# Kernel tuning notes

Hardware: AMD Instinct MI355X
Metric: run time of the kernel (lower is better)

## Reference

```python
import jax, jax.numpy as jnp
import numpy as np

N = 4096; E = 4096
IN_DIM = 256; H1 = 128; H2 = 128; H3 = 64; OUT = 16
NH1 = 2; NH2 = 2; ALPHA = 0.2
TDIMS = [933, 303, 683, 798]  # per-timepoint raw dims (nomal_linear1..4)
TP = 4; GRU_IN = 2 * OUT; GRU_H = 128


def _leaky(x, s):
    return jnp.where(x >= 0, x, s * x)


def _att_layer(x, mask, W, a, b):
    # GAT-style: h = xW; e = leaky(Wh1 + Wh2^T); adjacency-masked softmax; aggregate
    h = x @ W                                   # [N, d]
    d = W.shape[-1]
    e = _leaky((h @ a[:d])[:, None] + (h @ a[d:])[None, :], ALPHA)  # [N, N]
    att = jax.nn.softmax(jnp.where(mask, e, -9e15), axis=1)
    out = _leaky(att @ h, ALPHA)
    out = out / jnp.maximum(jnp.linalg.norm(out, axis=1, keepdims=True), 1e-12)
    return out + b

_multi_head = jax.vmap(_att_layer, in_axes=(None, None, 0, 0, 0))


def _encode(x, mask, W1, a1, b1, W2, a2, b2):
    x = jax.nn.elu(jnp.mean(_multi_head(x, mask, W1, a1, b1), axis=0))
    # second conv layer runs under torch.no_grad() in the original
    return jax.lax.stop_gradient(jnp.mean(_multi_head(x, mask, W2, a2, b2), axis=0))


def _gru_layer(xs, wih, whh, bih, bhh):
    # xs: [T, B, in]; torch GRU gate order (r, z, n)
    B = xs.shape[1]
    def step(h, xt):
        gi = xt @ wih + bih
        gh = h @ whh + bhh
        ir, iz, inn = jnp.split(gi, 3, axis=-1)
        hr, hz, hn = jnp.split(gh, 3, axis=-1)
        r = jax.nn.sigmoid(ir + hr)
        z = jax.nn.sigmoid(iz + hz)
        n = jnp.tanh(inn + r * hn)
        h_new = (1.0 - z) * n + z * h
        return h_new, h_new
    _, ys = jax.lax.scan(step, jnp.zeros((B, GRU_H), xs.dtype), xs)
    return ys


def setup_inputs() -> dict:
    key = jax.random.key(0)
    ks = iter(jax.random.split(key, 80))
    def rn(shape, s=0.05):
        return jax.random.normal(next(ks), shape, dtype=jnp.float32) * s
    inp = {}
    for i, d in enumerate(TDIMS):
        inp['x%d' % i] = rn((N, d), 1.0)
    inp['adj'] = jax.random.randint(next(ks), (N, N), 0, 2, dtype=jnp.int32)
    inp['train_sample'] = jax.random.randint(next(ks), (E, 2), 0, N)
    for i, d in enumerate(TDIMS):
        inp['nw%d' % i] = rn((d, IN_DIM))
        inp['nb%d' % i] = jnp.zeros((IN_DIM,), jnp.float32)
    inp['W1'] = rn((NH1, IN_DIM, H1)); inp['a1'] = rn((NH1, 2 * H1)); inp['b1'] = jnp.zeros((NH1, H1), jnp.float32)
    inp['W2'] = rn((NH2, H1, H2));     inp['a2'] = rn((NH2, 2 * H2)); inp['b2'] = jnp.zeros((NH2, H2), jnp.float32)
    inp['tfw1'] = rn((H2, H3)); inp['tfb1'] = jnp.zeros((H3,), jnp.float32)
    inp['tfw2'] = rn((H3, OUT)); inp['tfb2'] = jnp.zeros((OUT,), jnp.float32)
    inp['tgw1'] = rn((H2, H3)); inp['tgb1'] = jnp.zeros((H3,), jnp.float32)
    inp['tgw2'] = rn((H3, OUT)); inp['tgb2'] = jnp.zeros((OUT,), jnp.float32)
    inp['wih0'] = rn((GRU_IN, 3 * GRU_H)); inp['whh0'] = rn((GRU_H, 3 * GRU_H))
    inp['bih0'] = jnp.zeros((3 * GRU_H,), jnp.float32); inp['bhh0'] = jnp.zeros((3 * GRU_H,), jnp.float32)
    inp['wih1'] = rn((GRU_H, 3 * GRU_H)); inp['whh1'] = rn((GRU_H, 3 * GRU_H))
    inp['bih1'] = jnp.zeros((3 * GRU_H,), jnp.float32); inp['bhh1'] = jnp.zeros((3 * GRU_H,), jnp.float32)
    inp['attw'] = rn((GRU_H, GRU_H)); inp['attb'] = jnp.zeros((GRU_H,), jnp.float32)
    inp['fow'] = rn((GRU_H, 1)); inp['fob'] = jnp.zeros((1,), jnp.float32)
    return inp


def reference(x0, x1, x2, x3, adj, train_sample,
              nw0, nb0, nw1, nb1, nw2, nb2, nw3, nb3,
              W1, a1, b1, W2, a2, b2,
              tfw1, tfb1, tfw2, tfb2, tgw1, tgb1, tgw2, tgb2,
              wih0, whh0, bih0, bhh0, wih1, whh1, bih1, bhh1,
              attw, attb, fow, fob):
    mask = adj > 0
    xs = (x0, x1, x2, x3)
    nws = ((nw0, nb0), (nw1, nb1), (nw2, nb2), (nw3, nb3))
    tf_idx = train_sample[:, 0]
    tg_idx = train_sample[:, 1]
    steps = []
    for i in range(TP):  # fixed small loop over time points
        w, b = nws[i]
        e = xs[i] @ w + b                       # per-timepoint projection to input_dim
        embed = _encode(e, mask, W1, a1, b1, W2, a2, b2)
        # dropout (p=0.01) treated as identity for a deterministic reference
        tf = _leaky(_leaky(embed @ tfw1 + tfb1, 0.01) @ tfw2 + tfb2, 0.01)
        tg = _leaky(_leaky(embed @ tgw1 + tgb1, 0.01) @ tgw2 + tgb2, 0.01)
        steps.append(jnp.concatenate([tf[tf_idx], tg[tg_idx]], axis=1))  # [E, 32]
    h_x = jnp.stack(steps, axis=0)              # [T, E, 32]
    y0 = _gru_layer(h_x, wih0, whh0, bih0, bhh0)            # [T, E, 128]
    r_out = jnp.transpose(_gru_layer(y0, wih1, whh1, bih1, bhh1), (1, 0, 2))  # [E, T, 128]
    aw = jax.nn.softmax(r_out @ attw + attb, axis=1)        # softmax over time dim
    att_out = jnp.sum(aw * r_out, axis=1)                   # [E, 128]
    return att_out @ fow + fob                              # [E, 1]
```

## Files before the change

### kernel.cpp

```cpp
#include <hip/hip_runtime.h>
#include <cstdint>
#include <cstddef>

#define NN 4096
#define DH 128
#define TP 4
#define ATT_S 4
#define ATT_BM 64

typedef _Float16 f16x8 __attribute__((ext_vector_type(8)));
typedef float f32x4 __attribute__((ext_vector_type(4)));

__global__ __launch_bounds__(256) void pack_mask_k(const int* __restrict__ adj,
                                                   unsigned long long* __restrict__ mb) {
  int w = blockIdx.x * 4 + (threadIdx.x >> 6);
  int lane = threadIdx.x & 63;
  int v = adj[(size_t)w * 64 + lane];
  unsigned long long bits = __ballot(v > 0);
  if (lane == 0) mb[w] = bits;
}

template <int ACT, int BHEAD>
__global__ __launch_bounds__(256) void gemm_mfma_k(const float* __restrict__ A, const float* __restrict__ B,
                                                   const float* __restrict__ bias, float* __restrict__ C,
                                                   int M, int N, int K) {
  __shared__ _Float16 AH[64 * 64], AL[64 * 64];
  __shared__ _Float16 BH[64 * 64], BL[64 * 64];
  const int tid = threadIdx.x;
  const int bm = blockIdx.y * 64, bn = blockIdx.x * 64;
  const int arow = tid >> 2, akc = (tid & 3) * 16;
  const int bcol = tid & 63, bkc = (tid >> 6) * 16;
  const int w = tid >> 6, lane = tid & 63;
  const int wm = w >> 1, wn = w & 1;
  const int l15 = lane & 15, l4 = lane >> 4;
  f32x4 acc[2][2] = {};

  const float* Bp = B;
  int bcb = bn;
  if (BHEAD) { int hd = bn >> 7; Bp = B + (size_t)hd * K * 128; bcb = bn & 127; }
  const int ldb = BHEAD ? 128 : N;

  for (int k0 = 0; k0 < K; k0 += 64) {
    __syncthreads();
    {
      const float* ar = A + (size_t)(bm + arow) * K;
      f16x8 hv[2], lv[2];
#pragma unroll
      for (int e = 0; e < 16; e++) {
        int gk = k0 + akc + e;
        float v = (gk < K) ? ar[gk] : 0.f;
        _Float16 hi = (_Float16)v;
        hv[e >> 3][e & 7] = hi;
        lv[e >> 3][e & 7] = (_Float16)(v - (float)hi);
      }
#pragma unroll
      for (int hf = 0; hf < 2; hf++) {
        int byt = ((arow * 64 + akc + hf * 8) * 2) ^ ((arow & 7) << 4);
        *(f16x8*)((char*)AH + byt) = hv[hf];
        *(f16x8*)((char*)AL + byt) = lv[hf];
      }
    }
    {
      f16x8 hv[2], lv[2];
      const bool cok = (bcb + bcol) < ldb;
#pragma unroll
      for (int e = 0; e < 16; e++) {
        int gk = k0 + bkc + e;
        float v = (gk < K && cok) ? Bp[(size_t)gk * ldb + bcb + bcol] : 0.f;
        _Float16 hi = (_Float16)v;
        hv[e >> 3][e & 7] = hi;
        lv[e >> 3][e & 7] = (_Float16)(v - (float)hi);
      }
#pragma unroll
      for (int hf = 0; hf < 2; hf++) {
        int byt = ((bcol * 64 + bkc + hf * 8) * 2) ^ ((bcol & 7) << 4);
        *(f16x8*)((char*)BH + byt) = hv[hf];
        *(f16x8*)((char*)BL + byt) = lv[hf];
      }
    }
    __syncthreads();
#pragma unroll
    for (int kf = 0; kf < 2; kf++) {
      f16x8 ah[2], al[2], bh[2], bl[2];
#pragma unroll
      for (int m2 = 0; m2 < 2; m2++) {
        int r = wm * 32 + m2 * 16 + l15;
        int byt = ((r * 64 + kf * 32 + l4 * 8) * 2) ^ ((r & 7) << 4);
        ah[m2] = *(const f16x8*)((const char*)AH + byt);
        al[m2] = *(const f16x8*)((const char*)AL + byt);
      }
#pragma unroll
      for (int nf = 0; nf < 2; nf++) {
        int c = wn * 32 + nf * 16 + l15;
        int byt = ((c * 64 + kf * 32 + l4 * 8) * 2) ^ ((c & 7) << 4);
        bh[nf] = *(const f16x8*)((const char*)BH + byt);
        bl[nf] = *(const f16x8*)((const char*)BL + byt);
      }
#pragma unroll
      for (int m2 = 0; m2 < 2; m2++)
#pragma unroll
        for (int nf = 0; nf < 2; nf++) {
          acc[m2][nf] = __builtin_amdgcn_mfma_f32_16x16x32_f16(ah[m2], bh[nf], acc[m2][nf], 0, 0, 0);
          acc[m2][nf] = __builtin_amdgcn_mfma_f32_16x16x32_f16(ah[m2], bl[nf], acc[m2][nf], 0, 0, 0);
          acc[m2][nf] = __builtin_amdgcn_mfma_f32_16x16x32_f16(al[m2], bh[nf], acc[m2][nf], 0, 0, 0);
        }
    }
  }
#pragma unroll
  for (int m2 = 0; m2 < 2; m2++)
#pragma unroll
    for (int nf = 0; nf < 2; nf++) {
      int c = bn + wn * 32 + nf * 16 + l15;
      if (c < N) {
        float bv = bias ? bias[c] : 0.f;
#pragma unroll
        for (int q = 0; q < 4; q++) {
          int r = bm + wm * 32 + m2 * 16 + l4 * 4 + q;
          float v = acc[m2][nf][q] + bv;
          if (ACT == 1) v = (v >= 0.f) ? v : 0.01f * v;
          C[(size_t)r * N + c] = v;
        }
      }
    }
}

__global__ __launch_bounds__(256) void eler_k(const float* __restrict__ hcat, const float* __restrict__ a,
                                              float* __restrict__ el, float* __restrict__ er) {
  int head = blockIdx.y;
  const float* ah = a + (size_t)head * 256;
  int row = blockIdx.x * 4 + (threadIdx.x >> 6);
  int lane = threadIdx.x & 63;
  const float* hr = hcat + (size_t)row * 256 + head * 128;
  float h0 = hr[lane], h1 = hr[lane + 64];
  float pe = h0 * ah[lane] + h1 * ah[lane + 64];
  float pr = h0 * ah[128 + lane] + h1 * ah[192 + lane];
#pragma unroll
  for (int off = 32; off >= 1; off >>= 1) {
    pe += __shfl_xor(pe, off, 64);
    pr += __shfl_xor(pr, off, 64);
  }
  if (lane == 0) { el[(size_t)head * NN + row] = pe; er[(size_t)head * NN + row] = pr; }
}

__global__ __launch_bounds__(256) void rowmax_k(const float* __restrict__ el, const float* __restrict__ er,
                                                const unsigned long long* __restrict__ mb,
                                                float* __restrict__ mrow) {
  int head = blockIdx.y;
  int row = blockIdx.x * 4 + (threadIdx.x >> 6);
  int lane = threadIdx.x & 63;
  const float* erh = er + (size_t)head * NN;
  const unsigned long long* mr = mb + (size_t)row * 64;
  float mx = -INFINITY;
  for (int i = 0; i < 64; i++) {
    unsigned long long w = mr[i];
    float v = erh[i * 64 + lane];
    mx = fmaxf(mx, ((w >> lane) & 1ull) ? v : -INFINITY);
  }
#pragma unroll
  for (int off = 32; off >= 1; off >>= 1) mx = fmaxf(mx, __shfl_xor(mx, off, 64));
  if (lane == 0) {
    float s = el[(size_t)head * NN + row] + mx;
    mrow[(size_t)head * NN + row] = fmaxf(s, 0.2f * s);
  }
}

__global__ __launch_bounds__(256) void hsplit_k(const float* __restrict__ hcat,
                                                _Float16* __restrict__ HTH, _Float16* __restrict__ HTL) {
  const int jblk = blockIdx.x;
  const int head = blockIdx.y;
  const int tid = threadIdx.x;
  const int c = tid & 127;
  const size_t tileBase = ((size_t)head * (NN / 64) + jblk) * 8192;
#pragma unroll
  for (int kq = 0; kq < 4; kq++) {
    int k0 = (tid >> 7) * 32 + kq * 8;
    f16x8 hv, lv;
#pragma unroll
    for (int e = 0; e < 8; e++) {
      float v = hcat[(size_t)(jblk * 64 + k0 + e) * 256 + head * 128 + c];
      _Float16 hi = (_Float16)v;
      hv[e] = hi;
      lv[e] = (_Float16)(v - (float)hi);
    }
    int byt = ((c * 64 + k0) * 2) ^ ((c & 7) << 4);
    *(f16x8*)((char*)(HTH + tileBase) + byt) = hv;
    *(f16x8*)((char*)(HTL + tileBase) + byt) = lv;
  }
}

__global__ __launch_bounds__(256) void gat_mfma_k(const _Float16* __restrict__ HTH_g,
                                                  const _Float16* __restrict__ HTL_g,
                                                  const float* __restrict__ el, const float* __restrict__ er,
                                                  const float* __restrict__ mrow,
                                                  const unsigned long long* __restrict__ mb,
                                                  float* __restrict__ Opart, float* __restrict__ Zpart) {
  const int split = blockIdx.x;
  const int mblk = blockIdx.y;
  const int head = blockIdx.z;
  const float* elh = el + (size_t)head * NN;
  const float* erh = er + (size_t)head * NN;
  const float* mh = mrow + (size_t)head * NN;
  float* Op = Opart + ((size_t)head * ATT_S + split) * NN * DH;
  float* Zp = Zpart + ((size_t)head * ATT_S + split) * NN;

  __shared__ _Float16 PH[ATT_BM * 64];
  __shared__ _Float16 PL[ATT_BM * 64];
  __shared__ _Float16 HH[128 * 64];
  __shared__ _Float16 HL[128 * 64];
  __shared__ float zred[ATT_BM][4];

  const int tid = threadIdx.x;
  const int prow = tid >> 2;
  const int pk0 = (tid & 3) * 16;
  const int grow = mblk * ATT_BM + prow;
  const float el_r = elh[grow];
  const float m_r = mh[grow];
  const int w = tid >> 6, lane = tid & 63;
  const int wm = w >> 1, wn = w & 1;
  const int l15 = lane & 15, l4 = lane >> 4;

  f32x4 acc[2][4] = {};
  float zacc = 0.f;
  const int jbase = split * (NN / ATT_S);

  for (int jt = 0; jt < NN / ATT_S; jt += 64) {
    const int j0 = jbase + jt;
    const int jblk = j0 >> 6;
    const char* srcH = (const char*)(HTH_g + ((size_t)head * (NN / 64) + jblk) * 8192);
    const char* srcL = (const char*)(HTL_g + ((size_t)head * (NN / 64) + jblk) * 8192);
    __syncthreads();

    f16x8 rh[4], rl[4];
#pragma unroll
    for (int i = 0; i < 4; i++) {
      rh[i] = *(const f16x8*)(srcH + (tid + i * 256) * 16);
      rl[i] = *(const f16x8*)(srcL + (tid + i * 256) * 16);
    }

    {
      unsigned long long wbits = mb[(size_t)grow * 64 + jblk];
      float er_v[16];
#pragma unroll
      for (int q = 0; q < 4; q++) {
        float4 t = *(const float4*)&erh[j0 + pk0 + q * 4];
        er_v[q * 4 + 0] = t.x; er_v[q * 4 + 1] = t.y;
        er_v[q * 4 + 2] = t.z; er_v[q * 4 + 3] = t.w;
      }
      f16x8 hv[2], lv[2];
#pragma unroll
      for (int e = 0; e < 16; e++) {
        float sr = el_r + er_v[e];
        float s = fmaxf(sr, 0.2f * sr);
        float p = ((wbits >> (pk0 + e)) & 1ull) ? __expf(s - m_r) : 0.f;
        zacc += p;
        _Float16 hi = (_Float16)p;
        hv[e >> 3][e & 7] = hi;
        lv[e >> 3][e & 7] = (_Float16)(p - (float)hi);
      }
#pragma unroll
      for (int half = 0; half < 2; half++) {
        int byt = (((prow * 64) + pk0 + half * 8) * 2) ^ ((prow & 7) << 4);
        *(f16x8*)((char*)PH + byt) = hv[half];
        *(f16x8*)((char*)PL + byt) = lv[half];
      }
    }

#pragma unroll
    for (int i = 0; i < 4; i++) {
      *(f16x8*)((char*)HH + (tid + i * 256) * 16) = rh[i];
      *(f16x8*)((char*)HL + (tid + i * 256) * 16) = rl[i];
    }
    __syncthreads();

#pragma unroll
    for (int kf = 0; kf < 2; kf++) {
      f16x8 ah[2], al[2];
#pragma unroll
      for (int m2 = 0; m2 < 2; m2++) {
        int ar = wm * 32 + m2 * 16 + l15;
        int ak = kf * 32 + l4 * 8;
        int ab = ((ar * 64 + ak) * 2) ^ ((ar & 7) << 4);
        ah[m2] = *(const f16x8*)((const char*)PH + ab);
        al[m2] = *(const f16x8*)((const char*)PL + ab);
      }
#pragma unroll
      for (int nf = 0; nf < 4; nf++) {
        int bc = wn * 64 + nf * 16 + l15;
        int bk = kf * 32 + l4 * 8;
        int bb = ((bc * 64 + bk) * 2) ^ ((bc & 7) << 4);
        f16x8 bh = *(const f16x8*)((const char*)HH + bb);
        f16x8 bl = *(const f16x8*)((const char*)HL + bb);
#pragma unroll
        for (int m2 = 0; m2 < 2; m2++) {
          acc[m2][nf] = __builtin_amdgcn_mfma_f32_16x16x32_f16(ah[m2], bh, acc[m2][nf], 0, 0, 0);
          acc[m2][nf] = __builtin_amdgcn_mfma_f32_16x16x32_f16(ah[m2], bl, acc[m2][nf], 0, 0, 0);
          acc[m2][nf] = __builtin_amdgcn_mfma_f32_16x16x32_f16(al[m2], bh, acc[m2][nf], 0, 0, 0);
        }
      }
    }
  }

  zred[prow][tid & 3] = zacc;
  __syncthreads();
  if (tid < ATT_BM) {
    float z = zred[tid][0] + zred[tid][1] + zred[tid][2] + zred[tid][3];
    Zp[mblk * ATT_BM + tid] = z;
  }

#pragma unroll
  for (int m2 = 0; m2 < 2; m2++)
#pragma unroll
    for (int nf = 0; nf < 4; nf++)
#pragma unroll
      for (int q = 0; q < 4; q++) {
        int r = mblk * ATT_BM + wm * 32 + m2 * 16 + l4 * 4 + q;
        int c = wn * 64 + nf * 16 + l15;
        Op[(size_t)r * DH + c] = acc[m2][nf][q];
      }
}

template <int DO_ELU>
__global__ __launch_bounds__(256) void combine_k(const float* __restrict__ Opart,
                                                 const float* __restrict__ Zpart,
                                                 const float* __restrict__ bvec,
                                                 float* __restrict__ out) {
  int row = blockIdx.x * 4 + (threadIdx.x >> 6);
  int lane = threadIdx.x & 63;
  int c = lane * 2;
  float o0 = 0.f, o1 = 0.f;
#pragma unroll
  for (int hd = 0; hd < 2; hd++) {
    float a0 = 0.f, a1 = 0.f, Z = 0.f;
#pragma unroll
    for (int s = 0; s < ATT_S; s++) {
      const float* Op = Opart + ((size_t)hd * ATT_S + s) * NN * DH;
      float2 t = *(const float2*)&Op[(size_t)row * DH + c];
      a0 += t.x; a1 += t.y;
      Z += Zpart[((size_t)hd * ATT_S + s) * NN + row];
    }
    float invZ = 1.f / Z;
    float v0 = a0 * invZ, v1 = a1 * invZ;
    v0 = fmaxf(v0, 0.2f * v0);
    v1 = fmaxf(v1, 0.2f * v1);
    float ss = v0 * v0 + v1 * v1;
#pragma unroll
    for (int off = 32; off >= 1; off >>= 1) ss += __shfl_xor(ss, off, 64);
    float sc_ = 1.f / fmaxf(sqrtf(ss), 1e-12f);
    o0 += 0.5f * (v0 * sc_ + bvec[hd * DH + c]);
    o1 += 0.5f * (v1 * sc_ + bvec[hd * DH + c + 1]);
  }
  if (DO_ELU) {
    o0 = (o0 > 0.f) ? o0 : expm1f(o0);
    o1 = (o1 > 0.f) ? o1 : expm1f(o1);
  }
  float2 st = {o0, o1};
  *(float2*)&out[(size_t)row * DH + c] = st;
}

__global__ __launch_bounds__(256) void gather_k(const float* __restrict__ tf, const float* __restrict__ tg,
                                                const int* __restrict__ ts, float* __restrict__ hx_t) {
  int idx = blockIdx.x * 256 + threadIdx.x;
  int e = idx >> 5, c = idx & 31;
  int src = (c < 16) ? ts[e * 2] : ts[e * 2 + 1];
  float v = (c < 16) ? tf[(size_t)src * 16 + c] : tg[(size_t)src * 16 + (c - 16)];
  hx_t[idx] = v;
}

__global__ __launch_bounds__(256) void gru_gate_k(const float* __restrict__ gi, const float* __restrict__ gh,
                                                  const float* __restrict__ hprev, float* __restrict__ hout) {
  int idx = blockIdx.x * 256 + threadIdx.x;
  int b = idx >> 7, c = idx & 127;
  const float* gib = gi + (size_t)b * 384;
  const float* ghb = gh + (size_t)b * 384;
  float ir = gib[c], iz = gib[128 + c], in_ = gib[256 + c];
  float hr = ghb[c], hz = ghb[128 + c], hn = ghb[256 + c];
  float rr = 1.f / (1.f + __expf(-(ir + hr)));
  float zz = 1.f / (1.f + __expf(-(iz + hz)));
  float nn_ = tanhf(in_ + rr * hn);
  hout[idx] = (1.f - zz) * nn_ + zz * hprev[idx];
}

__global__ __launch_bounds__(256) void gru_gate0_k(const float* __restrict__ gi, const float* __restrict__ bhh,
                                                   float* __restrict__ hout) {
  int idx = blockIdx.x * 256 + threadIdx.x;
  int b = idx >> 7, c = idx & 127;
  const float* gib = gi + (size_t)b * 384;
  float ir = gib[c], iz = gib[128 + c], in_ = gib[256 + c];
  float hr = bhh[c], hz = bhh[128 + c], hn = bhh[256 + c];
  float rr = 1.f / (1.f + __expf(-(ir + hr)));
  float zz = 1.f / (1.f + __expf(-(iz + hz)));
  float nn_ = tanhf(in_ + rr * hn);
  hout[idx] = (1.f - zz) * nn_;
}

__global__ __launch_bounds__(256) void attpool_k(const float* __restrict__ z, const float* __restrict__ y,
                                                 float* __restrict__ o) {
  int idx = blockIdx.x * 256 + threadIdx.x;
  const size_t S = (size_t)NN * DH;
  float z0 = z[idx], z1 = z[idx + S], z2 = z[idx + 2 * S], z3 = z[idx + 3 * S];
  float mx = fmaxf(fmaxf(z0, z1), fmaxf(z2, z3));
  float e0 = __expf(z0 - mx), e1 = __expf(z1 - mx), e2 = __expf(z2 - mx), e3 = __expf(z3 - mx);
  float inv = 1.f / (e0 + e1 + e2 + e3);
  o[idx] = (e0 * y[idx] + e1 * y[idx + S] + e2 * y[idx + 2 * S] + e3 * y[idx + 3 * S]) * inv;
}

__global__ __launch_bounds__(256) void final_k(const float* __restrict__ at, const float* __restrict__ fow,
                                               const float* __restrict__ fob, float* __restrict__ out) {
  int row = blockIdx.x * 4 + (threadIdx.x >> 6);
  int lane = threadIdx.x & 63;
  const float* ar = at + (size_t)row * DH;
  float p = ar[lane] * fow[lane] + ar[lane + 64] * fow[lane + 64];
#pragma unroll
  for (int off = 32; off >= 1; off >>= 1) p += __shfl_xor(p, off, 64);
  if (lane == 0) out[row] = p + fob[0];
}

static inline void run_gemm(int act, const float* A, const float* B, const float* bias, float* C,
                            int M, int N, int K, hipStream_t s) {
  dim3 g((N + 63) / 64, M / 64), b(256);
  if (act == 0) gemm_mfma_k<0, 0><<<g, b, 0, s>>>(A, B, bias, C, M, N, K);
  else          gemm_mfma_k<1, 0><<<g, b, 0, s>>>(A, B, bias, C, M, N, K);
}
static inline void run_proj(const float* A, const float* B, float* C, int K, hipStream_t s) {
  gemm_mfma_k<0, 1><<<dim3(4, NN / 64), 256, 0, s>>>(A, B, nullptr, C, NN, 256, K);
}

extern "C" void kernel_launch(void* const* d_in, const int* in_sizes, int n_in,
                              void* d_out, int out_size, void* d_ws, size_t ws_size,
                              hipStream_t stream) {
  const float* x[4]  = {(const float*)d_in[0], (const float*)d_in[1], (const float*)d_in[2], (const float*)d_in[3]};
  const int* adj     = (const int*)d_in[4];
  const int* tsample = (const int*)d_in[5];
  const float* nw[4] = {(const float*)d_in[6], (const float*)d_in[8], (const float*)d_in[10], (const float*)d_in[12]};
  const float* nb[4] = {(const float*)d_in[7], (const float*)d_in[9], (const float*)d_in[11], (const float*)d_in[13]};
  const float* W1 = (const float*)d_in[14];
  const float* a1 = (const float*)d_in[15];
  const float* b1 = (const float*)d_in[16];
  const float* W2 = (const float*)d_in[17];
  const float* a2 = (const float*)d_in[18];
  const float* b2 = (const float*)d_in[19];
  const float* tfw1 = (const float*)d_in[20]; const float* tfb1 = (const float*)d_in[21];
  const float* tfw2 = (const float*)d_in[22]; const float* tfb2 = (const float*)d_in[23];
  const float* tgw1 = (const float*)d_in[24]; const float* tgb1 = (const float*)d_in[25];
  const float* tgw2 = (const float*)d_in[26]; const float* tgb2 = (const float*)d_in[27];
  const float* wih0 = (const float*)d_in[28]; const float* whh0 = (const float*)d_in[29];
  const float* bih0 = (const float*)d_in[30]; const float* bhh0 = (const float*)d_in[31];
  const float* wih1 = (const float*)d_in[32]; const float* whh1 = (const float*)d_in[33];
  const float* bih1 = (const float*)d_in[34]; const float* bhh1 = (const float*)d_in[35];
  const float* attw = (const float*)d_in[36]; const float* attb = (const float*)d_in[37];
  const float* fow  = (const float*)d_in[38]; const float* fob  = (const float*)d_in[39];
  float* out = (float*)d_out;

  char* base = (char*)d_ws;
  size_t off = 0;
  auto alloc = [&](size_t bytes) -> void* {
    void* p = base + off;
    off += (bytes + 255) & ~(size_t)255;
    return p;
  };
  const size_t SN = (size_t)NN * DH;
  unsigned long long* mbits = (unsigned long long*)alloc((size_t)NN * 64 * 8);
  float* ebuf = (float*)alloc((size_t)NN * 256 * 4);
  float* hcat = (float*)alloc((size_t)NN * 256 * 4);
  float* el   = (float*)alloc((size_t)2 * NN * 4);
  float* er   = (float*)alloc((size_t)2 * NN * 4);
  float* mrowb= (float*)alloc((size_t)2 * NN * 4);
  float* bufA = (float*)alloc(SN * 4);
  float* bufB = (float*)alloc(SN * 4);
  float* tmp1 = (float*)alloc((size_t)NN * 64 * 4);
  float* tfb_ = (float*)alloc((size_t)NN * 16 * 4);
  float* tgb_ = (float*)alloc((size_t)NN * 16 * 4);
  float* hx   = (float*)alloc((size_t)TP * NN * 32 * 4);
  float* y0   = (float*)alloc((size_t)TP * SN * 4);
  float* y1   = (float*)alloc((size_t)TP * SN * 4);
  float* gi   = (float*)alloc((size_t)NN * 384 * 4);
  float* gh   = (float*)alloc((size_t)NN * 384 * 4);
  float* Opart = y0;
  float* Zpart = gi;
  float* zatt   = gi;
  float* attout = hcat;
  _Float16* HTH = (_Float16*)ebuf;
  _Float16* HTL = HTH + (size_t)2 * NN * 128;

  const int TD[4] = {933, 303, 683, 798};

  pack_mask_k<<<(NN * 64) / 4, 256, 0, stream>>>(adj, mbits);

  for (int t = 0; t < TP; t++) {
    run_gemm(0, x[t], nw[t], nb[t], ebuf, NN, 256, TD[t], stream);

    run_proj(ebuf, W1, hcat, 256, stream);
    hsplit_k<<<dim3(NN / 64, 2), 256, 0, stream>>>(hcat, HTH, HTL);
    eler_k<<<dim3(NN / 4, 2), 256, 0, stream>>>(hcat, a1, el, er);
    rowmax_k<<<dim3(NN / 4, 2), 256, 0, stream>>>(el, er, mbits, mrowb);
    gat_mfma_k<<<dim3(ATT_S, NN / ATT_BM, 2), 256, 0, stream>>>(HTH, HTL, el, er, mrowb, mbits, Opart, Zpart);
    combine_k<1><<<NN / 4, 256, 0, stream>>>(Opart, Zpart, b1, bufB);

    run_proj(bufB, W2, hcat, 128, stream);
    hsplit_k<<<dim3(NN / 64, 2), 256, 0, stream>>>(hcat, HTH, HTL);
    eler_k<<<dim3(NN / 4, 2), 256, 0, stream>>>(hcat, a2, el, er);
    rowmax_k<<<dim3(NN / 4, 2), 256, 0, stream>>>(el, er, mbits, mrowb);
    gat_mfma_k<<<dim3(ATT_S, NN / ATT_BM, 2), 256, 0, stream>>>(HTH, HTL, el, er, mrowb, mbits, Opart, Zpart);
    combine_k<0><<<NN / 4, 256, 0, stream>>>(Opart, Zpart, b2, bufA);

    run_gemm(1, bufA, tfw1, tfb1, tmp1, NN, 64, DH, stream);
    run_gemm(1, tmp1, tfw2, tfb2, tfb_, NN, 16, 64, stream);
    run_gemm(1, bufA, tgw1, tgb1, tmp1, NN, 64, DH, stream);
    run_gemm(1, tmp1, tgw2, tgb2, tgb_, NN, 16, 64, stream);
    gather_k<<<(NN * 32) / 256, 256, 0, stream>>>(tfb_, tgb_, tsample, hx + (size_t)t * NN * 32);
  }

  run_gemm(0, hx, wih0, bih0, gi, NN, 384, 32, stream);
  gru_gate0_k<<<(int)(SN / 256), 256, 0, stream>>>(gi, bhh0, y0);
  for (int t = 1; t < TP; t++) {
    const float* hprev = y0 + (size_t)(t - 1) * SN;
    run_gemm(0, hx + (size_t)t * NN * 32, wih0, bih0, gi, NN, 384, 32, stream);
    run_gemm(0, hprev, whh0, bhh0, gh, NN, 384, DH, stream);
    gru_gate_k<<<(int)(SN / 256), 256, 0, stream>>>(gi, gh, hprev, y0 + (size_t)t * SN);
  }
  run_gemm(0, y0, wih1, bih1, gi, NN, 384, DH, stream);
  gru_gate0_k<<<(int)(SN / 256), 256, 0, stream>>>(gi, bhh1, y1);
  for (int t = 1; t < TP; t++) {
    const float* hprev = y1 + (size_t)(t - 1) * SN;
    run_gemm(0, y0 + (size_t)t * SN, wih1, bih1, gi, NN, 384, DH, stream);
    run_gemm(0, hprev, whh1, bhh1, gh, NN, 384, DH, stream);
    gru_gate_k<<<(int)(SN / 256), 256, 0, stream>>>(gi, gh, hprev, y1 + (size_t)t * SN);
  }

  run_gemm(0, y1, attw, attb, zatt, TP * NN, DH, DH, stream);
  attpool_k<<<(int)(SN / 256), 256, 0, stream>>>(zatt, y1, attout);
  final_k<<<NN / 4, 256, 0, stream>>>(attout, fow, fob, out);
}
```

Before: 1.356 ms.

## Split-K input projection GEMM and halve GAT attention row tile

The per-timepoint input projection (K up to 933) now runs as a split-K GEMM over 256-wide K chunks, writing partial sums that a separate reduction kernel adds together with the bias. The goal is more blocks in flight for a skinny output (N=256). The GAT attention kernel drops its row tile from 64 to 32, with 8 threads per row and one 16-row MFMA fragment per wave, which doubles the grid for better occupancy and load balance. The costs are extra global traffic for the partial buffers plus a reduction launch, and in the attention kernel the H tile is reloaded for every 32-row block, so its reuse is halved.

Measured after the change: 1.366 ms. No clear change (+0.8%).

```diff
diff --git a/kernel.cpp b/kernel.cpp
--- a/kernel.cpp
+++ b/kernel.cpp
@@ -6,7 +6,7 @@
 #define DH 128
 #define TP 4
 #define ATT_S 4
-#define ATT_BM 64
+#define ATT_BM 32
 
 typedef _Float16 f16x8 __attribute__((ext_vector_type(8)));
 typedef float f32x4 __attribute__((ext_vector_type(4)));
@@ -124,6 +124,112 @@
     }
 }
 
+__global__ __launch_bounds__(256) void gemm_ksplit_k(const float* __restrict__ A, const float* __restrict__ B,
+                                                     float* __restrict__ Cpart, int M, int N, int K) {
+  __shared__ _Float16 AH[64 * 64], AL[64 * 64];
+  __shared__ _Float16 BH[64 * 64], BL[64 * 64];
+  const int tid = threadIdx.x;
+  const int bm = blockIdx.y * 64, bn = blockIdx.x * 64;
+  const int kbeg = blockIdx.z * 256;
+  const int kend = min(K, kbeg + 256);
+  float* C = Cpart + (size_t)blockIdx.z * M * N;
+  const int arow = tid >> 2, akc = (tid & 3) * 16;
+  const int bcol = tid & 63, bkc = (tid >> 6) * 16;
+  const int w = tid >> 6, lane = tid & 63;
+  const int wm = w >> 1, wn = w & 1;
+  const int l15 = lane & 15, l4 = lane >> 4;
+  f32x4 acc[2][2] = {};
+
+  for (int k0 = kbeg; k0 < kend; k0 += 64) {
+    __syncthreads();
+    {
+      const float* ar = A + (size_t)(bm + arow) * K;
+      f16x8 hv[2], lv[2];
+#pragma unroll
+      for (int e = 0; e < 16; e++) {
+        int gk = k0 + akc + e;
+        float v = (gk < K) ? ar[gk] : 0.f;
+        _Float16 hi = (_Float16)v;
+        hv[e >> 3][e & 7] = hi;
+        lv[e >> 3][e & 7] = (_Float16)(v - (float)hi);
+      }
+#pragma unroll
+      for (int hf = 0; hf < 2; hf++) {
+        int byt = ((arow * 64 + akc + hf * 8) * 2) ^ ((arow & 7) << 4);
+        *(f16x8*)((char*)AH + byt) = hv[hf];
+        *(f16x8*)((char*)AL + byt) = lv[hf];
+      }
+    }
+    {
+      f16x8 hv[2], lv[2];
+      const bool cok = (bn + bcol) < N;
+#pragma unroll
+      for (int e = 0; e < 16; e++) {
+        int gk = k0 + bkc + e;
+        float v = (gk < K && cok) ? B[(size_t)gk * N + bn + bcol] : 0.f;
+        _Float16 hi = (_Float16)v;
+        hv[e >> 3][e & 7] = hi;
+        lv[e >> 3][e & 7] = (_Float16)(v - (float)hi);
+      }
+#pragma unroll
+      for (int hf = 0; hf < 2; hf++) {
+        int byt = ((bcol * 64 + bkc + hf * 8) * 2) ^ ((bcol & 7) << 4);
+        *(f16x8*)((char*)BH + byt) = hv[hf];
+        *(f16x8*)((char*)BL + byt) = lv[hf];
+      }
+    }
+    __syncthreads();
+#pragma unroll
+    for (int kf = 0; kf < 2; kf++) {
+      f16x8 ah[2], al[2], bh[2], bl[2];
+#pragma unroll
+      for (int m2 = 0; m2 < 2; m2++) {
+        int r = wm * 32 + m2 * 16 + l15;
+        int byt = ((r * 64 + kf * 32 + l4 * 8) * 2) ^ ((r & 7) << 4);
+        ah[m2] = *(const f16x8*)((const char*)AH + byt);
+        al[m2] = *(const f16x8*)((const char*)AL + byt);
+      }
+#pragma unroll
+      for (int nf = 0; nf < 2; nf++) {
+        int c = wn * 32 + nf * 16 + l15;
+        int byt = ((c * 64 + kf * 32 + l4 * 8) * 2) ^ ((c & 7) << 4);
+        bh[nf] = *(const f16x8*)((const char*)BH + byt);
+        bl[nf] = *(const f16x8*)((const char*)BL + byt);
+      }
+#pragma unroll
+      for (int m2 = 0; m2 < 2; m2++)
+#pragma unroll
+        for (int nf = 0; nf < 2; nf++) {
+          acc[m2][nf] = __builtin_amdgcn_mfma_f32_16x16x32_f16(ah[m2], bh[nf], acc[m2][nf], 0, 0, 0);
+          acc[m2][nf] = __builtin_amdgcn_mfma_f32_16x16x32_f16(ah[m2], bl[nf], acc[m2][nf], 0, 0, 0);
+          acc[m2][nf] = __builtin_amdgcn_mfma_f32_16x16x32_f16(al[m2], bh[nf], acc[m2][nf], 0, 0, 0);
+        }
+    }
+  }
+#pragma unroll
+  for (int m2 = 0; m2 < 2; m2++)
+#pragma unroll
+    for (int nf = 0; nf < 2; nf++) {
+      int c = bn + wn * 32 + nf * 16 + l15;
+      if (c < N) {
+#pragma unroll
+        for (int q = 0; q < 4; q++) {
+          int r = bm + wm * 32 + m2 * 16 + l4 * 4 + q;
+          C[(size_t)r * N + c] = acc[m2][nf][q];
+        }
+      }
+    }
+}
+
+__global__ __launch_bounds__(256) void ksum_k(const float* __restrict__ part, const float* __restrict__ bias,
+                                              float* __restrict__ C, int KS) {
+  int idx = blockIdx.x * 256 + threadIdx.x;
+  const size_t MN = (size_t)NN * 256;
+  float s = bias[idx & 255];
+  for (int i = 0; i < KS; i++) s += part[(size_t)i * MN + idx];
+  C[idx] = s;
+}
+
 __global__ __launch_bounds__(256) void eler_k(const float* __restrict__ hcat, const float* __restrict__ a,
                                               float* __restrict__ el, float* __restrict__ er) {
   int head = blockIdx.y;
@@ -207,11 +313,10 @@
   __shared__ _Float16 PL[ATT_BM * 64];
   __shared__ _Float16 HH[128 * 64];
   __shared__ _Float16 HL[128 * 64];
-  __shared__ float zred[ATT_BM][4];
 
   const int tid = threadIdx.x;
-  const int prow = tid >> 2;
-  const int pk0 = (tid & 3) * 16;
+  const int prow = tid >> 3;
+  const int pk0 = (tid & 7) * 8;
   const int grow = mblk * ATT_BM + prow;
   const float el_r = elh[grow];
   const float m_r = mh[grow];
@@ -219,7 +324,7 @@
   const int wm = w >> 1, wn = w & 1;
   const int l15 = lane & 15, l4 = lane >> 4;
 
-  f32x4 acc[2][4] = {};
+  f32x4 acc[4] = {};
   float zacc = 0.f;
   const int jbase = split * (NN / ATT_S);
 
@@ -239,30 +344,25 @@
 
     {
       unsigned long long wbits = mb[(size_t)grow * 64 + jblk];
-      float er_v[16];
-#pragma unroll
-      for (int q = 0; q < 4; q++) {
-        float4 t = *(const float4*)&erh[j0 + pk0 + q * 4];
-        er_v[q * 4 + 0] = t.x; er_v[q * 4 + 1] = t.y;
-        er_v[q * 4 + 2] = t.z; er_v[q * 4 + 3] = t.w;
-      }
-      f16x8 hv[2], lv[2];
-#pragma unroll
-      for (int e = 0; e < 16; e++) {
+      float er_v[8];
+      float4 t0 = *(const float4*)&erh[j0 + pk0];
+      float4 t1 = *(const float4*)&erh[j0 + pk0 + 4];
+      er_v[0] = t0.x; er_v[1] = t0.y; er_v[2] = t0.z; er_v[3] = t0.w;
+      er_v[4] = t1.x; er_v[5] = t1.y; er_v[6] = t1.z; er_v[7] = t1.w;
+      f16x8 hv, lv;
+#pragma unroll
+      for (int e = 0; e < 8; e++) {
         float sr = el_r + er_v[e];
         float s = fmaxf(sr, 0.2f * sr);
         float p = ((wbits >> (pk0 + e)) & 1ull) ? __expf(s - m_r) : 0.f;
         zacc += p;
         _Float16 hi = (_Float16)p;
-        hv[e >> 3][e & 7] = hi;
-        lv[e >> 3][e & 7] = (_Float16)(p - (float)hi);
-      }
-#pragma unroll
-      for (int half = 0; half < 2; half++) {
-        int byt = (((prow * 64) + pk0 + half * 8) * 2) ^ ((prow & 7) << 4);
-        *(f16x8*)((char*)PH + byt) = hv[half];
-        *(f16x8*)((char*)PL + byt) = lv[half];
-      }
+        hv[e] = hi;
+        lv[e] = (_Float16)(p - (float)hi);
+      }
+      int byt = (((prow * 64) + pk0) * 2) ^ ((prow & 7) << 4);
+      *(f16x8*)((char*)PH + byt) = hv;
+      *(f16x8*)((char*)PL + byt) = lv;
     }
 
 #pragma unroll
@@ -274,49 +374,42 @@
 
 #pragma unroll
     for (int kf = 0; kf < 2; kf++) {
-      f16x8 ah[2], al[2];
-#pragma unroll
-      for (int m2 = 0; m2 < 2; m2++) {
-        int ar = wm * 32 + m2 * 16 + l15;
-        int ak = kf * 32 + l4 * 8;
-        int ab = ((ar * 64 + ak) * 2) ^ ((ar & 7) << 4);
-        ah[m2] = *(const f16x8*)((const char*)PH + ab);
-        al[m2] = *(const f16x8*)((const char*)PL + ab);
-      }
+      int r = wm * 16 + l15;
+      int ab = ((r * 64 + kf * 32 + l4 * 8) * 2) ^ ((r & 7) << 4);
+      f16x8 ah = *(const f16x8*)((const char*)PH + ab);
+      f16x8 al = *(const f16x8*)((const char*)PL + ab);
 #pragma unroll
       for (int nf = 0; nf < 4; nf++) {
         int bc = wn * 64 + nf * 16 + l15;
-        int bk = kf * 32 + l4 * 8;
-        int bb = ((bc * 64 + bk) * 2) ^ ((bc & 7) << 4);
+        int bb = ((bc * 64 + kf * 32 + l4 * 8) * 2) ^ ((bc & 7) << 4);
         f16x8 bh = *(const f16x8*)((const char*)HH + bb);
         f16x8 bl = *(const f16x8*)((const char*)HL + bb);
-#pragma unroll
-        for (int m2 = 0; m2 < 2; m2++) {
-          acc[m2][nf] = __builtin_amdgcn_mfma_f32_16x16x32_f16(ah[m2], bh, acc[m2][nf], 0, 0, 0);
-          acc[m2][nf] = __builtin_amdgcn_mfma_f32_16x16x32_f16(ah[m2], bl, acc[m2][nf], 0, 0, 0);
-          acc[m2][nf] = __builtin_amdgcn_mfma_f32_16x16x32_f16(al[m2], bh, acc[m2][nf], 0, 0, 0);
-        }
-      }
-    }
-  }
-
-  zred[prow][tid & 3] = zacc;
+        acc[nf] = __builtin_amdgcn_mfma_f32_16x16x32_f16(ah, bh, acc[nf], 0, 0, 0);
+        acc[nf] = __builtin_amdgcn_mfma_f32_16x16x32_f16(ah, bl, acc[nf], 0, 0, 0);
+        acc[nf] = __builtin_amdgcn_mfma_f32_16x16x32_f16(al, bh, acc[nf], 0, 0, 0);
+      }
+    }
+  }
+
+  __syncthreads();
+  float* zred = (float*)PH;
+  zred[prow * 8 + (tid & 7)] = zacc;
   __syncthreads();
   if (tid < ATT_BM) {
-    float z = zred[tid][0] + zred[tid][1] + zred[tid][2] + zred[tid][3];
+    float z = 0.f;
+#pragma unroll
+    for (int i = 0; i < 8; i++) z += zred[tid * 8 + i];
     Zp[mblk * ATT_BM + tid] = z;
   }
 
 #pragma unroll
-  for (int m2 = 0; m2 < 2; m2++)
-#pragma unroll
-    for (int nf = 0; nf < 4; nf++)
-#pragma unroll
-      for (int q = 0; q < 4; q++) {
-        int r = mblk * ATT_BM + wm * 32 + m2 * 16 + l4 * 4 + q;
-        int c = wn * 64 + nf * 16 + l15;
-        Op[(size_t)r * DH + c] = acc[m2][nf][q];
-      }
+  for (int nf = 0; nf < 4; nf++)
+#pragma unroll
+    for (int q = 0; q < 4; q++) {
+      int r = mblk * ATT_BM + wm * 16 + l4 * 4 + q;
+      int c = wn * 64 + nf * 16 + l15;
+      Op[(size_t)r * DH + c] = acc[nf][q];
+    }
 }
 
 template <int DO_ELU>
@@ -476,6 +569,7 @@
   float* gi   = (float*)alloc((size_t)NN * 384 * 4);
   float* gh   = (float*)alloc((size_t)NN * 384 * 4);
   float* Opart = y0;
+  float* kpart = y0;
   float* Zpart = gi;
   float* zatt   = gi;
   float* attout = hcat;
@@ -487,7 +581,9 @@
   pack_mask_k<<<(NN * 64) / 4, 256, 0, stream>>>(adj, mbits);
 
   for (int t = 0; t < TP; t++) {
-    run_gemm(0, x[t], nw[t], nb[t], ebuf, NN, 256, TD[t], stream);
+    int KS = (TD[t] + 255) / 256;
+    gemm_ksplit_k<<<dim3(4, NN / 64, KS), 256, 0, stream>>>(x[t], nw[t], kpart, NN, 256, TD[t]);
+    ksum_k<<<(NN * 256) / 256, 256, 0, stream>>>(kpart, nb[t], ebuf, KS);
 
     run_proj(ebuf, W1, hcat, 256, stream);
     hsplit_k<<<dim3(NN / 64, 2), 256, 0, stream>>>(hcat, HTH, HTL);
```
